# Optimization experiments

Measured on AMD Instinct MI355X. Metric: run time of the kernel, lower is better.

Reference implementation:

```python
import jax, jax.numpy as jnp
import numpy as np

BIN_RES = 0.01
NUM_BINS = 512
T0 = 0.0
DECAY = 2.0
SCALE = 0.05
N = 131072


def setup_inputs() -> dict:
    key = jax.random.key(0)
    k1, k2, k3, k4, k5, k6 = jax.random.split(key, 6)
    means = jax.random.normal(k1, (N, 3), dtype=jnp.float32)
    scan_point = jax.random.normal(k2, (3,), dtype=jnp.float32)
    # parameters initialized near their nn.Parameter defaults with small noise
    colours = 0.1 + 0.05 * jax.random.normal(k3, (N, 1), dtype=jnp.float32)
    coefficients = 0.1 * jax.random.normal(k4, (N, 1), dtype=jnp.float32)
    opacities = 0.1 * jax.random.normal(k5, (N, 1), dtype=jnp.float32)
    pre_act_scales = jnp.log(jnp.float32(SCALE)) + 0.1 * jax.random.normal(k6, (N, 1), dtype=jnp.float32)
    return {
        "means": means,
        "scan_point": scan_point,
        "colours": colours,
        "coefficients": coefficients,
        "opacities": opacities,
        "pre_act_scales": pre_act_scales,
        "view_id": 0,
    }


def reference(means, scan_point, colours, coefficients, opacities, pre_act_scales, view_id):
    # render_conf_hist2 (confocal=True path)
    intensity = jax.nn.sigmoid(opacities[:, view_id]) * (colours[:, 0] ** 2)  # [N]
    coeff = jax.nn.sigmoid(coefficients)  # [N,1]
    r0 = jnp.linalg.norm(means - scan_point[None, :], axis=1, keepdims=True)  # [N,1]
    r_ = T0 / 2 + (BIN_RES / 2) * jnp.arange(1, 1 + NUM_BINS, dtype=jnp.float32)  # [B]
    r = r_[None, :]  # [1,B]
    sigma = jnp.mean(jnp.exp(pre_act_scales), axis=1, keepdims=True)  # [N,1]
    sigma = jnp.clip(sigma, BIN_RES / 2)  # lower clip only
    d = r - r0  # [N,B]
    g = jnp.exp(-0.5 * (d / sigma) ** 2)  # [N,B]
    pdf1 = np.sqrt(0.5 / np.pi) * g / sigma
    pdf2 = d * g / (sigma ** 2)
    pdf = coeff * pdf1 + (1.0 - coeff) * pdf2
    pr = jnp.clip(pdf * (BIN_RES / 2), 0.0, 1.0)  # [N,B]
    hist = jnp.sum(intensity[:, None] * pr, axis=0)  # [B]
    hist = hist / jnp.power(r_, DECAY)
    return hist
```

## Files before the change

kernel.cpp:

```cpp
#include <hip/hip_runtime.h>
#include <math.h>

#define NBINS 512
#define K1_THREADS 256

__global__ __launch_bounds__(K1_THREADS) void gauss_scatter(
    const float* __restrict__ means,
    const float* __restrict__ scan_point,
    const float* __restrict__ colours,
    const float* __restrict__ coefficients,
    const float* __restrict__ opacities,
    const float* __restrict__ pre_act,
    const int*   __restrict__ view_id_p,
    float* __restrict__ partial,
    int n)
{
    __shared__ float hist[NBINS];
    const int tid = threadIdx.x;
    hist[tid]       = 0.0f;
    hist[tid + 256] = 0.0f;
    __syncthreads();

    const int i = blockIdx.x * K1_THREADS + tid;
    if (i < n) {
        const int vid = view_id_p[0];
        const float op  = opacities[i + vid];
        const float col = colours[i];
        const float inten = (1.0f / (1.0f + __expf(-op))) * col * col;
        const float cf    = 1.0f / (1.0f + __expf(-coefficients[i]));

        const float dx = means[3*i]   - scan_point[0];
        const float dy = means[3*i+1] - scan_point[1];
        const float dz = means[3*i+2] - scan_point[2];
        const float r0 = sqrtf(fmaf(dx, dx, fmaf(dy, dy, dz*dz)));

        const float sigma = fmaxf(__expf(pre_act[i]), 0.005f);

        const float q  = 0.8493218002880191f / sigma;
        const float c  = inten * 0.005f;
        const float A2 = c * cf * 0.3989422804014327f / sigma;
        const float B3 = c * (1.0f - cf) / (0.8493218002880191f * sigma);

        const float rlo = r0 - (cf / (1.0f - cf)) * 0.3989422804014327f * sigma;
        const float rhi = r0 + 7.5f * sigma;
        int blo = (int)ceilf(rlo * 200.0f - 1.0f);
        int bhi = (int)floorf(rhi * 200.0f - 1.0f);
        blo = max(blo, 0);
        bhi = min(bhi, NBINS - 1);

        float e = (0.005f * (float)(blo + 1) - r0) * q;
        const float de = 0.005f * q;
        for (int b = blo; b <= bhi; ++b) {
            const float g = __builtin_amdgcn_exp2f(-(e * e));
            const float t = g * fmaf(B3, e, A2);
            unsafeAtomicAdd(&hist[b], t);
            e += de;
        }
    }
    __syncthreads();

    float* out = partial + (size_t)blockIdx.x * NBINS;
    out[tid]       = hist[tid];
    out[tid + 256] = hist[tid + 256];
}

__global__ __launch_bounds__(256) void gauss_reduce(
    const float* __restrict__ partial, float* __restrict__ out, int G)
{
    const int b = blockIdx.x;
    const int k = threadIdx.x;
    float s = 0.0f;
    for (int g = k; g < G; g += 256)
        s += partial[(size_t)g * NBINS + b];

    #pragma unroll
    for (int off = 32; off > 0; off >>= 1)
        s += __shfl_down(s, off, 64);

    __shared__ float wsum[4];
    if ((k & 63) == 0) wsum[k >> 6] = s;
    __syncthreads();
    if (k == 0) {
        const float t = wsum[0] + wsum[1] + wsum[2] + wsum[3];
        const float r = 0.005f * (float)(b + 1);
        out[b] = t / (r * r);
    }
}

extern "C" void kernel_launch(void* const* d_in, const int* in_sizes, int n_in,
                              void* d_out, int out_size, void* d_ws, size_t ws_size,
                              hipStream_t stream) {
    const float* means        = (const float*)d_in[0];
    const float* scan_point   = (const float*)d_in[1];
    const float* colours      = (const float*)d_in[2];
    const float* coefficients = (const float*)d_in[3];
    const float* opacities    = (const float*)d_in[4];
    const float* pre_act      = (const float*)d_in[5];
    const int*   view_id      = (const int*)d_in[6];

    const int n = in_sizes[2];
    const int G = (n + K1_THREADS - 1) / K1_THREADS;

    float* partial = (float*)d_ws;
    float* out = (float*)d_out;

    gauss_scatter<<<G, K1_THREADS, 0, stream>>>(
        means, scan_point, colours, coefficients, opacities, pre_act,
        view_id, partial, n);

    gauss_reduce<<<NBINS, 256, 0, stream>>>(partial, out, G);
}
```

Measured before the change: 21.47 us.

## Fuse reduction into scatter kernel via global atomics and larger blocks

Removes the separate reduction kernel and the per-block partial histogram buffer. Each block now scales its shared-memory histogram by 1/r^2 and adds only the nonzero bins into the output with global float atomics, after a memset zeroes the output. Blocks grow to 512 threads, so each thread owns one bin and there are half as many blocks. This trades a kernel launch and a round-trip through global memory for contention on global atomics over the few bins that receive contributions, and it makes the float summation order nondeterministic.

```diff
diff --git a/kernel.cpp b/kernel.cpp
--- a/kernel.cpp
+++ b/kernel.cpp
@@ -2,9 +2,9 @@
 #include <math.h>
 
 #define NBINS 512
-#define K1_THREADS 256
+#define K1_THREADS 512
 
-__global__ __launch_bounds__(K1_THREADS) void gauss_scatter(
+__global__ __launch_bounds__(K1_THREADS) void gauss_scatter_fused(
     const float* __restrict__ means,
     const float* __restrict__ scan_point,
     const float* __restrict__ colours,
@@ -12,13 +12,12 @@
     const float* __restrict__ opacities,
     const float* __restrict__ pre_act,
     const int*   __restrict__ view_id_p,
-    float* __restrict__ partial,
+    float* __restrict__ out,
     int n)
 {
     __shared__ float hist[NBINS];
     const int tid = threadIdx.x;
-    hist[tid]       = 0.0f;
-    hist[tid + 256] = 0.0f;
+    hist[tid] = 0.0f;
     __syncthreads();
 
     const int i = blockIdx.x * K1_THREADS + tid;
@@ -59,31 +58,10 @@
     }
     __syncthreads();
 
-    float* out = partial + (size_t)blockIdx.x * NBINS;
-    out[tid]       = hist[tid];
-    out[tid + 256] = hist[tid + 256];
-}
-
-__global__ __launch_bounds__(256) void gauss_reduce(
-    const float* __restrict__ partial, float* __restrict__ out, int G)
-{
-    const int b = blockIdx.x;
-    const int k = threadIdx.x;
-    float s = 0.0f;
-    for (int g = k; g < G; g += 256)
-        s += partial[(size_t)g * NBINS + b];
-
-    #pragma unroll
-    for (int off = 32; off > 0; off >>= 1)
-        s += __shfl_down(s, off, 64);
-
-    __shared__ float wsum[4];
-    if ((k & 63) == 0) wsum[k >> 6] = s;
-    __syncthreads();
-    if (k == 0) {
-        const float t = wsum[0] + wsum[1] + wsum[2] + wsum[3];
-        const float r = 0.005f * (float)(b + 1);
-        out[b] = t / (r * r);
+    const float v = hist[tid];
+    if (v != 0.0f) {
+        const float r = 0.005f * (float)(tid + 1);
+        unsafeAtomicAdd(&out[tid], v / (r * r));
     }
 }
 
@@ -101,12 +79,11 @@
     const int n = in_sizes[2];
     const int G = (n + K1_THREADS - 1) / K1_THREADS;
 
-    float* partial = (float*)d_ws;
     float* out = (float*)d_out;
 
-    gauss_scatter<<<G, K1_THREADS, 0, stream>>>(
+    hipMemsetAsync(out, 0, NBINS * sizeof(float), stream);
+
+    gauss_scatter_fused<<<G, K1_THREADS, 0, stream>>>(
         means, scan_point, colours, coefficients, opacities, pre_act,
-        view_id, partial, n);
-
-    gauss_reduce<<<NBINS, 256, 0, stream>>>(partial, out, G);
+        view_id, out, n);
 }
```

Result: slower. 23.63 us (+10.1%).
